# Kernel tuning notes

Measured on AMD Instinct MI355X. Metric: run time of the kernel, lower is better.

Reference implementation:

```python
import jax, jax.numpy as jnp
import numpy as np

BINS = 64
VMIN, VMAX = 0.0, 1.0
SIGMA = 0.02


def setup_inputs() -> dict:
    key = jax.random.key(0)
    x = jax.random.uniform(key, (8, 3, 512, 512), dtype=jnp.float32)
    centers = jnp.linspace(VMIN, VMAX, BINS, dtype=jnp.float32)
    return {"x": x, "centers": centers}


def reference(x, centers):
    B, C, H, W = x.shape
    xc = jnp.clip(x, VMIN, VMAX).reshape(B, C, H * W, 1)          # (B,C,P,1)
    c = centers.reshape(1, 1, 1, -1)                                # (1,1,1,bins)
    k = jnp.exp(-0.5 * ((xc - c) / (SIGMA + 1e-12)) ** 2)           # (B,C,P,bins)
    k = k / (jnp.sum(k, axis=-1, keepdims=True) + 1e-12)            # per-pixel normalize
    hist = jnp.mean(k, axis=2)                                      # (B,C,bins)
    hist = hist / (jnp.sum(hist, axis=-1, keepdims=True) + 1e-12)   # per-image normalize
    return hist
```

## Files before the change

### kernel.cpp

```cpp
#include <hip/hip_runtime.h>


#define NQ      1024
#define NBINS   64
#define NIMG    24
#define IMG_PIX (512 * 512)
#define BPI     32
#define CNT_BLOCKS (NIMG * BPI)
#define TBL_BLOCKS (NQ / 4)

__global__ __launch_bounds__(256) void soft_hist_k1(
    const float* __restrict__ x, const float* __restrict__ centers,
    float* __restrict__ table, unsigned int* __restrict__ parts)
{
    const int bid = blockIdx.x;
    const int t   = threadIdx.x;

    if (bid < CNT_BLOCKS) {
        __shared__ unsigned int h[NQ];
        #pragma unroll
        for (int k = 0; k < NQ / 256; ++k) h[t + k * 256] = 0u;
        __syncthreads();

        const float4* x4 = (const float4*)x + (size_t)bid * (IMG_PIX / 4 / BPI);

        float4 v[8];
        #pragma unroll
        for (int r = 0; r < 8; ++r) v[r] = x4[r * 256 + t];

        #pragma unroll
        for (int r = 0; r < 8; ++r) {
            const float4 p = v[r];
            int q0 = (int)(p.x * (float)NQ); q0 = q0 < 0 ? 0 : (q0 > NQ - 1 ? NQ - 1 : q0);
            int q1 = (int)(p.y * (float)NQ); q1 = q1 < 0 ? 0 : (q1 > NQ - 1 ? NQ - 1 : q1);
            int q2 = (int)(p.z * (float)NQ); q2 = q2 < 0 ? 0 : (q2 > NQ - 1 ? NQ - 1 : q2);
            int q3 = (int)(p.w * (float)NQ); q3 = q3 < 0 ? 0 : (q3 > NQ - 1 ? NQ - 1 : q3);
            atomicAdd(&h[q0], 1u);
            atomicAdd(&h[q1], 1u);
            atomicAdd(&h[q2], 1u);
            atomicAdd(&h[q3], 1u);
        }
        __syncthreads();

        unsigned int* dst = parts + (size_t)bid * NQ;
        #pragma unroll
        for (int k = 0; k < NQ / 256; ++k) dst[t + k * 256] = h[t + k * 256];
    } else {
        const int lane = t & 63;
        const int q    = (bid - CNT_BLOCKS) * 4 + (t >> 6);
        const float cq = ((float)q + 0.5f) * (1.0f / (float)NQ);
        const float d  = (cq - centers[lane]) * 50.0f;
        const float e  = expf(-0.5f * d * d);
        float s = e;
        #pragma unroll
        for (int off = 32; off > 0; off >>= 1) s += __shfl_xor(s, off, 64);
        table[q * NBINS + lane] = e / (s + 1e-12f);
    }
}

__global__ __launch_bounds__(256) void soft_hist_final(
    const unsigned int* __restrict__ parts, const float* __restrict__ table,
    float* __restrict__ out)
{
    __shared__ float tf[NQ];
    __shared__ float part[4][NBINS];
    const int t   = threadIdx.x;
    const int img = blockIdx.x;

    const unsigned int* src = parts + (size_t)img * BPI * NQ;
    #pragma unroll
    for (int k = 0; k < NQ / 256; ++k) {
        const int q = t + k * 256;
        unsigned int s = 0;
        #pragma unroll 8
        for (int b = 0; b < BPI; ++b) s += src[(size_t)b * NQ + q];
        tf[q] = (float)s;
    }
    __syncthreads();

    const int j  = t & 63;
    const int g  = t >> 6;
    const int Q4 = NQ / 4;
    float acc = 0.0f;
    const float* tb = table + (size_t)(g * Q4) * NBINS + j;
    #pragma unroll 4
    for (int qq = 0; qq < Q4; ++qq)
        acc += tb[(size_t)qq * NBINS] * tf[g * Q4 + qq];
    part[g][j] = acc;
    __syncthreads();

    if (t < 64) {
        const float hsum = part[0][t] + part[1][t] + part[2][t] + part[3][t];
        const float hm   = hsum * (1.0f / (float)IMG_PIX);
        float ss = hm;
        #pragma unroll
        for (int off = 32; off > 0; off >>= 1) ss += __shfl_xor(ss, off, 64);
        out[img * NBINS + t] = hm / (ss + 1e-12f);
    }
}

extern "C" void kernel_launch(void* const* d_in, const int* in_sizes, int n_in,
                              void* d_out, int out_size, void* d_ws, size_t ws_size,
                              hipStream_t stream)
{
    const float* x       = (const float*)d_in[0];
    const float* centers = (const float*)d_in[1];
    float* out           = (float*)d_out;

    float*        table = (float*)d_ws;
    unsigned int* parts = (unsigned int*)((char*)d_ws
                        + (size_t)NQ * NBINS * sizeof(float));

    soft_hist_k1<<<CNT_BLOCKS + TBL_BLOCKS, 256, 0, stream>>>(x, centers, table, parts);
    soft_hist_final<<<NIMG, 256, 0, stream>>>(parts, table, out);
}
```

Baseline: 89.98 us.

## Split final histogram reduction across quantization slices with last-block ticket combine

The final kernel, which ran only 24 blocks, now launches 8 blocks per image. Each block reduces one slice of the quantized-count space and computes that slice's partial contribution to the 64 bins. Partial bin sums go to a workspace buffer, and a per-image atomic ticket elects the last block to sum the slices and normalize. This spreads the serial partial-count reduction and table matvec over many more CUs, at the cost of an extra global round trip, fences and a ticket reset done in the first kernel.

```diff
diff --git a/kernel.cpp b/kernel.cpp
--- a/kernel.cpp
+++ b/kernel.cpp
@@ -8,10 +8,13 @@
 #define BPI     32
 #define CNT_BLOCKS (NIMG * BPI)
 #define TBL_BLOCKS (NQ / 4)
+#define SLICES  8
+#define SLICE_Q (NQ / SLICES)
 
 __global__ __launch_bounds__(256) void soft_hist_k1(
     const float* __restrict__ x, const float* __restrict__ centers,
-    float* __restrict__ table, unsigned int* __restrict__ parts)
+    float* __restrict__ table, unsigned int* __restrict__ parts,
+    unsigned int* __restrict__ tickets)
 {
     const int bid = blockIdx.x;
     const int t   = threadIdx.x;
@@ -46,6 +49,8 @@
         #pragma unroll
         for (int k = 0; k < NQ / 256; ++k) dst[t + k * 256] = h[t + k * 256];
     } else {
+        if (bid == CNT_BLOCKS && t < NIMG) tickets[t] = 0u;
+
         const int lane = t & 63;
         const int q    = (bid - CNT_BLOCKS) * 4 + (t >> 6);
         const float cq = ((float)q + 0.5f) * (1.0f / (float)NQ);
@@ -60,38 +65,60 @@
 
 __global__ __launch_bounds__(256) void soft_hist_final(
     const unsigned int* __restrict__ parts, const float* __restrict__ table,
-    float* __restrict__ out)
+    float* gpart, unsigned int* tickets, float* __restrict__ out)
 {
-    __shared__ float tf[NQ];
+    __shared__ float sh[2 * SLICE_Q];
+    __shared__ float tf[SLICE_Q];
     __shared__ float part[4][NBINS];
+    __shared__ unsigned int is_last;
+
     const int t   = threadIdx.x;
-    const int img = blockIdx.x;
+    const int img = blockIdx.x / SLICES;
+    const int k   = blockIdx.x % SLICES;
 
-    const unsigned int* src = parts + (size_t)img * BPI * NQ;
-    #pragma unroll
-    for (int k = 0; k < NQ / 256; ++k) {
-        const int q = t + k * 256;
+    {
+        const int c = t & (SLICE_Q - 1);
+        const int h = t >> 7;
+        const unsigned int* src = parts + (size_t)img * BPI * NQ
+                                 + (size_t)(h * 16) * NQ + (k * SLICE_Q + c);
         unsigned int s = 0;
-        #pragma unroll 8
-        for (int b = 0; b < BPI; ++b) s += src[(size_t)b * NQ + q];
-        tf[q] = (float)s;
+        #pragma unroll
+        for (int b = 0; b < 16; ++b) s += src[(size_t)b * NQ];
+        sh[h * SLICE_Q + c] = (float)s;
     }
     __syncthreads();
+    if (t < SLICE_Q) tf[t] = sh[t] + sh[SLICE_Q + t];
+    __syncthreads();
 
-    const int j  = t & 63;
-    const int g  = t >> 6;
-    const int Q4 = NQ / 4;
+    const int j = t & 63;
+    const int g = t >> 6;
     float acc = 0.0f;
-    const float* tb = table + (size_t)(g * Q4) * NBINS + j;
-    #pragma unroll 4
-    for (int qq = 0; qq < Q4; ++qq)
-        acc += tb[(size_t)qq * NBINS] * tf[g * Q4 + qq];
+    const float* tb = table + (size_t)(k * SLICE_Q + g * 32) * NBINS + j;
+    #pragma unroll
+    for (int qq = 0; qq < 32; ++qq)
+        acc += tb[(size_t)qq * NBINS] * tf[g * 32 + qq];
     part[g][j] = acc;
     __syncthreads();
 
-    if (t < 64) {
-        const float hsum = part[0][t] + part[1][t] + part[2][t] + part[3][t];
-        const float hm   = hsum * (1.0f / (float)IMG_PIX);
+    if (t < NBINS)
+        gpart[(size_t)(img * SLICES + k) * NBINS + t]
+            = part[0][t] + part[1][t] + part[2][t] + part[3][t];
+
+    __threadfence();
+    if (t == 0) {
+        const unsigned int old = atomicAdd(&tickets[img], 1u);
+        is_last = (old == SLICES - 1) ? 1u : 0u;
+    }
+    __syncthreads();
+    if (!is_last) return;
+    __threadfence();
+
+    if (t < NBINS) {
+        const float* gp = gpart + (size_t)img * SLICES * NBINS + t;
+        float hsum = 0.0f;
+        #pragma unroll
+        for (int kk = 0; kk < SLICES; ++kk) hsum += gp[(size_t)kk * NBINS];
+        const float hm = hsum * (1.0f / (float)IMG_PIX);
         float ss = hm;
         #pragma unroll
         for (int off = 32; off > 0; off >>= 1) ss += __shfl_xor(ss, off, 64);
@@ -107,10 +134,17 @@
     const float* centers = (const float*)d_in[1];
     float* out           = (float*)d_out;
 
-    float*        table = (float*)d_ws;
-    unsigned int* parts = (unsigned int*)((char*)d_ws
-                        + (size_t)NQ * NBINS * sizeof(float));
+    char* ws = (char*)d_ws;
+    float*        table   = (float*)ws;
+    ws += (size_t)NQ * NBINS * sizeof(float);
+    unsigned int* parts   = (unsigned int*)ws;
+    ws += (size_t)CNT_BLOCKS * NQ * sizeof(unsigned int);
+    float*        gpart   = (float*)ws;
+    ws += (size_t)NIMG * SLICES * NBINS * sizeof(float);
+    unsigned int* tickets = (unsigned int*)ws;
 
-    soft_hist_k1<<<CNT_BLOCKS + TBL_BLOCKS, 256, 0, stream>>>(x, centers, table, parts);
-    soft_hist_final<<<NIMG, 256, 0, stream>>>(parts, table, out);
+    soft_hist_k1<<<CNT_BLOCKS + TBL_BLOCKS, 256, 0, stream>>>(
+        x, centers, table, parts, tickets);
+    soft_hist_final<<<NIMG * SLICES, 256, 0, stream>>>(
+        parts, table, gpart, tickets, out);
 }
```

Measured after the change: 86.92 us. -3.4%, faster.

## Fuse histogram, kernel-table and final reduction into one kernel with ticket finalization

Applied to the files above, without the earlier changes.

Replaces the two-kernel pipeline with a single kernel. Each block builds its quantized count histogram, then applies a banded (16-bin) Gaussian kernel per quantization level directly in shared memory. The block adds its result into a global per-image accumulator, and the last-arriving block (via a ticket counter) normalizes and writes the output. This removes the second launch, the workspace table and the partial-count traffic. In exchange it adds global float atomics and truncates the Gaussian to a band. It also relies on persistent device globals that are reset only by the finalizing block.

```diff
diff --git a/kernel.cpp b/kernel.cpp
--- a/kernel.cpp
+++ b/kernel.cpp
@@ -7,91 +7,91 @@
 #define IMG_PIX (512 * 512)
 #define BPI     32
 #define CNT_BLOCKS (NIMG * BPI)
-#define TBL_BLOCKS (NQ / 4)
+#define BANDW   16
 
-__global__ __launch_bounds__(256) void soft_hist_k1(
+__device__ float        g_hist[NIMG * NBINS];
+__device__ unsigned int g_ticket[NIMG];
+
+__global__ __launch_bounds__(256) void soft_hist_fused(
     const float* __restrict__ x, const float* __restrict__ centers,
-    float* __restrict__ table, unsigned int* __restrict__ parts)
+    float* __restrict__ out)
 {
+    __shared__ unsigned int h[NQ];
+    __shared__ float        fh[NBINS];
+    __shared__ float        cl[NBINS];
+    __shared__ unsigned int s_last;
+
     const int bid = blockIdx.x;
     const int t   = threadIdx.x;
+    const int img = bid >> 5;
 
-    if (bid < CNT_BLOCKS) {
-        __shared__ unsigned int h[NQ];
-        #pragma unroll
-        for (int k = 0; k < NQ / 256; ++k) h[t + k * 256] = 0u;
-        __syncthreads();
+    #pragma unroll
+    for (int k = 0; k < NQ / 256; ++k) h[t + k * 256] = 0u;
+    if (t < NBINS) { fh[t] = 0.0f; cl[t] = centers[t]; }
+    __syncthreads();
 
-        const float4* x4 = (const float4*)x + (size_t)bid * (IMG_PIX / 4 / BPI);
+    const float4* x4 = (const float4*)x + (size_t)bid * (IMG_PIX / 4 / BPI);
+    float4 v[8];
+    #pragma unroll
+    for (int r = 0; r < 8; ++r) v[r] = x4[r * 256 + t];
 
-        float4 v[8];
-        #pragma unroll
-        for (int r = 0; r < 8; ++r) v[r] = x4[r * 256 + t];
-
-        #pragma unroll
-        for (int r = 0; r < 8; ++r) {
-            const float4 p = v[r];
-            int q0 = (int)(p.x * (float)NQ); q0 = q0 < 0 ? 0 : (q0 > NQ - 1 ? NQ - 1 : q0);
-            int q1 = (int)(p.y * (float)NQ); q1 = q1 < 0 ? 0 : (q1 > NQ - 1 ? NQ - 1 : q1);
-            int q2 = (int)(p.z * (float)NQ); q2 = q2 < 0 ? 0 : (q2 > NQ - 1 ? NQ - 1 : q2);
-            int q3 = (int)(p.w * (float)NQ); q3 = q3 < 0 ? 0 : (q3 > NQ - 1 ? NQ - 1 : q3);
-            atomicAdd(&h[q0], 1u);
-            atomicAdd(&h[q1], 1u);
-            atomicAdd(&h[q2], 1u);
-            atomicAdd(&h[q3], 1u);
-        }
-        __syncthreads();
-
-        unsigned int* dst = parts + (size_t)bid * NQ;
-        #pragma unroll
-        for (int k = 0; k < NQ / 256; ++k) dst[t + k * 256] = h[t + k * 256];
-    } else {
-        const int lane = t & 63;
-        const int q    = (bid - CNT_BLOCKS) * 4 + (t >> 6);
-        const float cq = ((float)q + 0.5f) * (1.0f / (float)NQ);
-        const float d  = (cq - centers[lane]) * 50.0f;
-        const float e  = expf(-0.5f * d * d);
-        float s = e;
-        #pragma unroll
-        for (int off = 32; off > 0; off >>= 1) s += __shfl_xor(s, off, 64);
-        table[q * NBINS + lane] = e / (s + 1e-12f);
-    }
-}
-
-__global__ __launch_bounds__(256) void soft_hist_final(
-    const unsigned int* __restrict__ parts, const float* __restrict__ table,
-    float* __restrict__ out)
-{
-    __shared__ float tf[NQ];
-    __shared__ float part[4][NBINS];
-    const int t   = threadIdx.x;
-    const int img = blockIdx.x;
-
-    const unsigned int* src = parts + (size_t)img * BPI * NQ;
     #pragma unroll
-    for (int k = 0; k < NQ / 256; ++k) {
-        const int q = t + k * 256;
-        unsigned int s = 0;
-        #pragma unroll 8
-        for (int b = 0; b < BPI; ++b) s += src[(size_t)b * NQ + q];
-        tf[q] = (float)s;
+    for (int r = 0; r < 8; ++r) {
+        const float4 p = v[r];
+        int q0 = (int)(p.x * (float)NQ); q0 = q0 < 0 ? 0 : (q0 > NQ - 1 ? NQ - 1 : q0);
+        int q1 = (int)(p.y * (float)NQ); q1 = q1 < 0 ? 0 : (q1 > NQ - 1 ? NQ - 1 : q1);
+        int q2 = (int)(p.z * (float)NQ); q2 = q2 < 0 ? 0 : (q2 > NQ - 1 ? NQ - 1 : q2);
+        int q3 = (int)(p.w * (float)NQ); q3 = q3 < 0 ? 0 : (q3 > NQ - 1 ? NQ - 1 : q3);
+        atomicAdd(&h[q0], 1u);
+        atomicAdd(&h[q1], 1u);
+        atomicAdd(&h[q2], 1u);
+        atomicAdd(&h[q3], 1u);
     }
     __syncthreads();
 
-    const int j  = t & 63;
-    const int g  = t >> 6;
-    const int Q4 = NQ / 4;
-    float acc = 0.0f;
-    const float* tb = table + (size_t)(g * Q4) * NBINS + j;
-    #pragma unroll 4
-    for (int qq = 0; qq < Q4; ++qq)
-        acc += tb[(size_t)qq * NBINS] * tf[g * Q4 + qq];
-    part[g][j] = acc;
+    {
+        const int lane = t & 63;
+        const int wv   = t >> 6;
+        #pragma unroll
+        for (int k = 0; k < 4; ++k) {
+            const int   q  = 16 * lane + 4 * wv + k;
+            const float n  = (float)h[q];
+            const float cq = ((float)q + 0.5f) * (1.0f / (float)NQ);
+            const int   jc = (int)(cq * 63.0f + 0.5f);
+            int js = jc - 7;
+            js = js < 0 ? 0 : (js > NBINS - BANDW ? NBINS - BANDW : js);
+            float e[BANDW];
+            float s = 1e-12f;
+            #pragma unroll
+            for (int i = 0; i < BANDW; ++i) {
+                const float d = (cq - cl[js + i]) * 50.0f;
+                e[i] = __expf(-0.5f * d * d);
+                s += e[i];
+            }
+            const float scale = n / s;
+            #pragma unroll
+            for (int i = 0; i < BANDW; ++i)
+                atomicAdd(&fh[js + i], e[i] * scale);
+        }
+    }
     __syncthreads();
 
-    if (t < 64) {
-        const float hsum = part[0][t] + part[1][t] + part[2][t] + part[3][t];
-        const float hm   = hsum * (1.0f / (float)IMG_PIX);
+    if (t < NBINS) {
+        const float old = atomicAdd(&g_hist[img * NBINS + t], fh[t]);
+        asm volatile("" :: "v"(old));
+    }
+    __syncthreads();
+
+    if (t == 0)
+        s_last = ((atomicAdd(&g_ticket[img], 1u) & 31u) == 31u) ? 1u : 0u;
+    __syncthreads();
+    if (!s_last) return;
+
+    if (t < NBINS) {
+        float* p = &g_hist[img * NBINS + t];
+        const float hsum = atomicAdd(p, 0.0f);
+        atomicExch(p, 0.0f);
+        const float hm = hsum * (1.0f / (float)IMG_PIX);
         float ss = hm;
         #pragma unroll
         for (int off = 32; off > 0; off >>= 1) ss += __shfl_xor(ss, off, 64);
@@ -106,11 +106,7 @@
     const float* x       = (const float*)d_in[0];
     const float* centers = (const float*)d_in[1];
     float* out           = (float*)d_out;
+    (void)d_ws; (void)ws_size;
 
-    float*        table = (float*)d_ws;
-    unsigned int* parts = (unsigned int*)((char*)d_ws
-                        + (size_t)NQ * NBINS * sizeof(float));
-
-    soft_hist_k1<<<CNT_BLOCKS + TBL_BLOCKS, 256, 0, stream>>>(x, centers, table, parts);
-    soft_hist_final<<<NIMG, 256, 0, stream>>>(parts, table, out);
+    soft_hist_fused<<<CNT_BLOCKS, 256, 0, stream>>>(x, centers, out);
 }
```

After: 137.9 us. 1.53x slower.
